# Kernel tuning notes

Measured on AMD Instinct MI355X. Metric: run time of the kernel, lower is better.

## Reference

```python
import jax, jax.numpy as jnp
import numpy as np

B, S, H = 1, 2048, 1024      # batch, seq, hidden_size
F = 4096                     # intermediate_size
E = 8                        # num_experts
K = 2                        # top-k routing


def setup_inputs() -> dict:
    key = jax.random.key(0)
    ks = jax.random.split(key, 7)
    s = 0.02  # init scale
    return {
        "x": jax.random.normal(ks[0], (B, S, H), jnp.float32),
        "gate_w": jax.random.normal(ks[1], (H, E), jnp.float32) * s,
        "gate_b": jnp.zeros((E,), jnp.float32),
        "w1": jax.random.normal(ks[2], (E, H, F), jnp.float32) * s,
        "b1": jnp.zeros((E, F), jnp.float32),
        "w2": jax.random.normal(ks[3], (E, F, H), jnp.float32) * s,
        "b2": jnp.zeros((E, H), jnp.float32),
    }


def reference(x, gate_w, gate_b, w1, b1, w2, b2):
    Bq, Sq, Hq = x.shape
    T = Bq * Sq
    xt = x.reshape(T, Hq)                              # [T,H] flatten tokens

    # --- router: softmax gate, top-k, renormalize top-k weights ---
    logits = xt @ gate_w + gate_b                      # [T,E]
    probs = jax.nn.softmax(logits, axis=-1)            # [T,E]
    top_v, top_i = jax.lax.top_k(probs, K)             # [T,K]
    top_v = top_v / jnp.sum(top_v, axis=-1, keepdims=True)
    combine = jnp.zeros((T, E), x.dtype).at[jnp.arange(T)[:, None], top_i].set(top_v)  # [T,E] sparse combine weights

    # --- experts: 2-layer FFN (ReLU), batched over experts ---
    h = jax.nn.relu(jnp.einsum('th,ehf->etf', xt, w1) + b1[:, None, :])   # [E,T,F]
    y = jnp.einsum('etf,efh->eth', h, w2) + b2[:, None, :]                # [E,T,H]

    # --- combine: weighted sum over selected experts (zeros elsewhere) ---
    out = jnp.einsum('te,eth->th', combine, y)          # [T,H]
    return out.reshape(Bq, Sq, Hq)
```

## Files before the change

kernel.cpp:

```cpp
#include <hip/hip_runtime.h>

#define TT 2048
#define HH 1024
#define FF 4096
#define EE 8
#define EROWS 640
#define ROWS_CAP 5120
#define KSPLIT2 4

typedef __bf16 bf16;
typedef bf16 bf16x8 __attribute__((ext_vector_type(8)));
typedef bf16 bf16x4 __attribute__((ext_vector_type(4)));
typedef bf16 bf16x2 __attribute__((ext_vector_type(2)));
typedef float floatx4 __attribute__((ext_vector_type(4)));

#define OFF_W1T  ((size_t)0)
#define OFF_W2T  (OFF_W1T + (size_t)67108864)
#define OFF_XG   (OFF_W2T + (size_t)67108864)
#define OFF_H    (OFF_XG  + (size_t)10485760)
#define OFF_CNT  (OFF_H   + (size_t)41943040)
#define OFF_TKW  (OFF_CNT + (size_t)256)
#define OFF_ROW  (OFF_TKW + (size_t)16384)
#define OFF_Y    OFF_W1T

__device__ __forceinline__ void gload16(const bf16* g, bf16* l) {
    __builtin_amdgcn_global_load_lds((const __attribute__((address_space(1))) void*)g,
                                     (__attribute__((address_space(3))) void*)l, 16, 0, 0);
}

__device__ __forceinline__ void raw_barrier() {
    asm volatile("s_barrier" ::: "memory");
}

__global__ __launch_bounds__(256) void transpose_cvt(const float* __restrict__ in,
                                                     bf16* __restrict__ out,
                                                     int R, int C) {
    __shared__ float tile[64][67];
    const int e  = blockIdx.z;
    const int r0 = blockIdx.y * 64, c0 = blockIdx.x * 64;
    const float* inp = in + (size_t)e * R * C;
    bf16* outp = out + (size_t)e * R * C;
    const int t = threadIdx.x;
    {
        const int lr = t >> 4;
        const int lc = (t & 15) << 2;
#pragma unroll
        for (int i = 0; i < 4; ++i) {
            int r = lr + i * 16;
            floatx4 v = __builtin_nontemporal_load(
                (const floatx4*)&inp[(size_t)(r0 + r) * C + c0 + lc]);
            tile[r][lc + 0] = v[0]; tile[r][lc + 1] = v[1];
            tile[r][lc + 2] = v[2]; tile[r][lc + 3] = v[3];
        }
    }
    __syncthreads();
    {
        const int c  = t >> 3;
        const int rq = (t & 7) << 3;
#pragma unroll
        for (int i = 0; i < 2; ++i) {
            int cc = c + i * 32;
            bf16x8 o;
#pragma unroll
            for (int k = 0; k < 8; ++k) o[k] = (bf16)tile[rq + k][cc];
            *(bf16x8*)&outp[(size_t)(c0 + cc) * R + r0 + rq] = o;
        }
    }
}

__global__ __launch_bounds__(256) void router_gather(const float* __restrict__ x,
                                                     const float* __restrict__ gw,
                                                     const float* __restrict__ gb,
                                                     int* __restrict__ counts,
                                                     bf16* __restrict__ xg,
                                                     int* __restrict__ rowOf,
                                                     float* __restrict__ tkw) {
    const int wid = blockIdx.x * 4 + (threadIdx.x >> 6);
    const int lane = threadIdx.x & 63;
    for (int t = wid; t < TT; t += 1024) {
        const float* xr = x + (size_t)t * HH;
        float xf[16];
        double acc[EE];
#pragma unroll
        for (int e = 0; e < EE; ++e) acc[e] = 0.0;
#pragma unroll
        for (int i = 0; i < 16; ++i) {
            const int h = lane + i * 64;
            const float xv = xr[h];
            xf[i] = xv;
            const float* g = gw + (size_t)h * EE;
            floatx4 g0 = *(const floatx4*)&g[0];
            floatx4 g1 = *(const floatx4*)&g[4];
            const double xd = (double)xv;
            acc[0] += xd * (double)g0[0]; acc[1] += xd * (double)g0[1];
            acc[2] += xd * (double)g0[2]; acc[3] += xd * (double)g0[3];
            acc[4] += xd * (double)g1[0]; acc[5] += xd * (double)g1[1];
            acc[6] += xd * (double)g1[2]; acc[7] += xd * (double)g1[3];
        }
#pragma unroll
        for (int e = 0; e < EE; ++e) {
            double v = acc[e];
            for (int s = 32; s > 0; s >>= 1) v += __shfl_xor(v, s, 64);
            acc[e] = v + (double)gb[e];
        }
        int row1 = 0, row2 = 0;
        if (lane == 0) {
            int i1 = 0; double v1 = acc[0];
            for (int e = 1; e < EE; ++e) if (acc[e] > v1) { v1 = acc[e]; i1 = e; }
            int i2 = -1; double v2 = -1e300;
            for (int e = 0; e < EE; ++e) if (e != i1 && acc[e] > v2) { v2 = acc[e]; i2 = e; }
            double wa = 1.0 / (1.0 + exp(v2 - v1));
            double wb = 1.0 - wa;
            int r1 = atomicAdd(&counts[i1], 1); if (r1 > EROWS - 1) r1 = EROWS - 1;
            int r2 = atomicAdd(&counts[i2], 1); if (r2 > EROWS - 1) r2 = EROWS - 1;
            row1 = i1 * EROWS + r1;
            row2 = i2 * EROWS + r2;
            rowOf[t * 2 + 0] = row1; rowOf[t * 2 + 1] = row2;
            tkw[t * 2 + 0] = (float)wa; tkw[t * 2 + 1] = (float)wb;
        }
        row1 = __shfl(row1, 0, 64);
        row2 = __shfl(row2, 0, 64);
        bf16* d1 = xg + (size_t)row1 * HH;
        bf16* d2 = xg + (size_t)row2 * HH;
#pragma unroll
        for (int i = 0; i < 16; ++i) {
            const bf16 v = (bf16)xf[i];
            d1[lane + i * 64] = v;
            d2[lane + i * 64] = v;
        }
    }
}


#define GEMM_BODY(EPILOGUE)                                                                 \
    __shared__ bf16 As[3][128 * 32];                                                        \
    __shared__ bf16 Bs[3][256 * 32];                                                        \
    const int tid = threadIdx.x;                                                            \
    const int lane = tid & 63, wave = tid >> 6;                                             \
    const int lrow = lane & 15, lq = lane >> 4;                                             \
    const int m_w = (wave & 1) << 6, n_w = (wave >> 1) << 7;                                \
    const unsigned foff = (unsigned)((lq ^ ((lrow >> 1) & 3)) << 3);                        \
    floatx4 acc[4][8];                                                                      \
    _Pragma("unroll") for (int i = 0; i < 4; ++i)                                           \
        _Pragma("unroll") for (int j = 0; j < 8; ++j)                                       \
            acc[i][j] = (floatx4){0.f, 0.f, 0.f, 0.f};                                      \
    int arow[6]; size_t gadr[6];                                                            \
    _Pragma("unroll") for (int s = 0; s < 6; ++s) {                                         \
        int c = tid + ((s < 2) ? s * 256 : (s - 2) * 256);                                  \
        int ar = c >> 2, ak = (c & 3) ^ ((ar >> 1) & 3);                                    \
        arow[s] = ar; gadr[s] = (size_t)ar * K + (size_t)ak * 8;                            \
    }                                                                                       \
    const unsigned ldsw = (unsigned)((tid & ~63) << 4);                \
                                                               \
    _Pragma("unroll") for (int p = 0; p < 2; ++p) {                                         \
        const int kb = p * 32;                                                              \
        gload16(Ab + gadr[0] + kb, (bf16*)((char*)As[p] + ldsw));                           \
        gload16(Ab + gadr[1] + kb, (bf16*)((char*)As[p] + 4096u + ldsw));                   \
        gload16(Bb + gadr[2] + kb, (bf16*)((char*)Bs[p] + ldsw));                           \
        gload16(Bb + gadr[3] + kb, (bf16*)((char*)Bs[p] + 4096u + ldsw));                   \
        gload16(Bb + gadr[4] + kb, (bf16*)((char*)Bs[p] + 8192u + ldsw));                   \
        gload16(Bb + gadr[5] + kb, (bf16*)((char*)Bs[p] + 12288u + ldsw));                  \
    }                                                                                       \
    for (int kt = 0; kt < NK; ++kt) {                                                       \
        raw_barrier();                              \
        {                                                                                   \
            const int kn = (kt + 2 < NK) ? kt + 2 : NK - 1;       \
            const int nb = (kt + 2) % 3;                                                    \
            const int kb = kn * 32;                                                         \
            gload16(Ab + gadr[0] + kb, (bf16*)((char*)As[nb] + ldsw));                      \
            gload16(Ab + gadr[1] + kb, (bf16*)((char*)As[nb] + 4096u + ldsw));              \
            gload16(Bb + gadr[2] + kb, (bf16*)((char*)Bs[nb] + ldsw));                      \
            gload16(Bb + gadr[3] + kb, (bf16*)((char*)Bs[nb] + 4096u + ldsw));              \
            gload16(Bb + gadr[4] + kb, (bf16*)((char*)Bs[nb] + 8192u + ldsw));              \
            gload16(Bb + gadr[5] + kb, (bf16*)((char*)Bs[nb] + 12288u + ldsw));             \
        }                                                                                   \
        asm volatile("s_waitcnt vmcnt(12)" ::: "memory");      \
        raw_barrier();                                               \
        const int cb = kt % 3;                                                              \
        bf16x8 af[4], bfr[8];                                                               \
        _Pragma("unroll") for (int i = 0; i < 4; ++i) {                                     \
            int m = m_w + i * 16 + lrow;                                                    \
            af[i] = *(const bf16x8*)&As[cb][(unsigned)m * 32 + foff];                       \
        }                                                                                   \
        _Pragma("unroll") for (int j = 0; j < 8; ++j) {                                     \
            int n = n_w + j * 16 + lrow;                                                    \
            bfr[j] = *(const bf16x8*)&Bs[cb][(unsigned)n * 32 + foff];                      \
        }                                                                                   \
        _Pragma("unroll") for (int i = 0; i < 4; ++i)                                       \
            _Pragma("unroll") for (int j = 0; j < 8; ++j)                                   \
                acc[i][j] = __builtin_amdgcn_mfma_f32_16x16x32_bf16(af[i], bfr[j],          \
                                                                    acc[i][j], 0, 0, 0);    \
    }                                                                                       \
    asm volatile("s_waitcnt vmcnt(0)" ::: "memory");           \
    EPILOGUE

__global__ __launch_bounds__(256, 2) void gemm1_kernel(const bf16* __restrict__ A,
                                                       const bf16* __restrict__ Bt,
                                                       const float* __restrict__ b1,
                                                       bf16* __restrict__ Hout,
                                                       const int* __restrict__ counts) {
    const int e = blockIdx.z, mt = blockIdx.y, nt = blockIdx.x;
    const int cnt = counts[e];
    if (mt * 128 >= cnt) return;
    const int row0 = e * EROWS + mt * 128;
    const int K = HH;
    const int NK = K / 32;
    const bf16* Ab = A + (size_t)row0 * K;
    const bf16* Bb = Bt + ((size_t)e * FF + (size_t)nt * 256) * K;

    GEMM_BODY({
        const float* bias = b1 + (size_t)e * FF + (size_t)nt * 256;
        bf16* Hb = Hout + (size_t)row0 * FF + (size_t)nt * 256;
        _Pragma("unroll") for (int j = 0; j < 8; ++j) {
            int col = n_w + j * 16 + lrow;
            float bv = bias[col];
            _Pragma("unroll") for (int i = 0; i < 4; ++i)
                _Pragma("unroll") for (int r = 0; r < 4; ++r) {
                    int mrow = m_w + i * 16 + (lq << 2) + r;
                    float v = acc[i][j][r] + bv;
                    Hb[(size_t)mrow * FF + col] = (bf16)(v > 0.f ? v : 0.f);
                }
        }
    })
}

__global__ __launch_bounds__(256, 2) void gemm2_kernel(const bf16* __restrict__ Hin,
                                                       const bf16* __restrict__ Bt,
                                                       const float* __restrict__ b2,
                                                       bf16* __restrict__ Y,
                                                       const int* __restrict__ counts) {
    const int e = blockIdx.z >> 2, ks = blockIdx.z & 3;
    const int mt = blockIdx.y, nt = blockIdx.x;
    const int cnt = counts[e];
    if (mt * 128 >= cnt) return;
    const int row0 = e * EROWS + mt * 128;
    const int K = FF;
    const int KC = FF / KSPLIT2;
    const int NK = KC / 32;
    const bf16* Ab = Hin + (size_t)row0 * K + ks * KC;
    const bf16* Bb = Bt + ((size_t)e * HH + (size_t)nt * 256) * K + ks * KC;

    GEMM_BODY({
        const float* bias = b2 + (size_t)e * HH + (size_t)nt * 256;
        bf16* Yb = Y + ((size_t)ks * ROWS_CAP + row0) * HH + (size_t)nt * 256;
        _Pragma("unroll") for (int j = 0; j < 8; ++j) {
            int col = n_w + j * 16 + lrow;
            float bv = (ks == 0) ? bias[col] : 0.f;
            _Pragma("unroll") for (int i = 0; i < 4; ++i)
                _Pragma("unroll") for (int r = 0; r < 4; ++r) {
                    int mrow = m_w + i * 16 + (lq << 2) + r;
                    Yb[(size_t)mrow * HH + col] = (bf16)(acc[i][j][r] + bv);
                }
        }
    })
}

__global__ __launch_bounds__(256) void combine_kernel(const bf16* __restrict__ Y,
                                                      const int* __restrict__ rowOf,
                                                      const float* __restrict__ tkw,
                                                      float* __restrict__ out) {
    const int t = blockIdx.x;
    const int tid = threadIdx.x;
    const int ra = rowOf[t * 2 + 0], rb = rowOf[t * 2 + 1];
    const float wa = tkw[t * 2 + 0], wb = tkw[t * 2 + 1];
    const int c = tid * 4;
    float acc[4] = {0.f, 0.f, 0.f, 0.f};
#pragma unroll
    for (int ks = 0; ks < KSPLIT2; ++ks) {
        bf16x4 a = *(const bf16x4*)&Y[((size_t)ks * ROWS_CAP + ra) * HH + c];
        bf16x4 b = *(const bf16x4*)&Y[((size_t)ks * ROWS_CAP + rb) * HH + c];
#pragma unroll
        for (int k = 0; k < 4; ++k) acc[k] += wa * (float)a[k] + wb * (float)b[k];
    }
    floatx4 o; o[0] = acc[0]; o[1] = acc[1]; o[2] = acc[2]; o[3] = acc[3];
    *(floatx4*)&out[(size_t)t * HH + c] = o;
}

extern "C" void kernel_launch(void* const* d_in, const int* in_sizes, int n_in,
                              void* d_out, int out_size, void* d_ws, size_t ws_size,
                              hipStream_t stream) {
    const float* x  = (const float*)d_in[0];
    const float* gw = (const float*)d_in[1];
    const float* gb = (const float*)d_in[2];
    const float* w1 = (const float*)d_in[3];
    const float* b1 = (const float*)d_in[4];
    const float* w2 = (const float*)d_in[5];
    const float* b2 = (const float*)d_in[6];
    float* out = (float*)d_out;
    char* ws = (char*)d_ws;

    bf16*  w1t  = (bf16*)(ws + OFF_W1T);
    bf16*  w2t  = (bf16*)(ws + OFF_W2T);
    bf16*  xg   = (bf16*)(ws + OFF_XG);
    bf16*  hbuf = (bf16*)(ws + OFF_H);
    bf16*  ybuf = (bf16*)(ws + OFF_Y);
    int*   cnts = (int*)(ws + OFF_CNT);
    float* tkw  = (float*)(ws + OFF_TKW);
    int*   rowOf= (int*)(ws + OFF_ROW);

    hipMemsetAsync(cnts, 0, 256, stream);

    router_gather<<<256, 256, 0, stream>>>(x, gw, gb, cnts, xg, rowOf, tkw);
    transpose_cvt<<<dim3(FF / 64, HH / 64, EE), 256, 0, stream>>>(w1, w1t, HH, FF);
    transpose_cvt<<<dim3(HH / 64, FF / 64, EE), 256, 0, stream>>>(w2, w2t, FF, HH);
    gemm1_kernel<<<dim3(FF / 256, 5, EE), 256, 0, stream>>>(xg, w1t, b1, hbuf, cnts);
    gemm2_kernel<<<dim3(HH / 256, 5, EE * KSPLIT2), 256, 0, stream>>>(hbuf, w2t, b2, ybuf, cnts);
    combine_kernel<<<TT, 256, 0, stream>>>(ybuf, rowOf, tkw, out);
}
```

Before: 492.1 us.

## Fuse fp32 weight transpose-convert into GEMM B-tile loading

Removes the two separate transpose_cvt kernels that converted fp32 w1/w2 to transposed bf16 in the workspace. Each GEMM now reads fp32 weights directly through registers, converts them to bf16 and writes them swizzled into LDS. The pipeline changes from a 3-stage async global_load_lds ring to a 2-stage register-prefetch double buffer with __syncthreads. This saves a full read and write pass over 512MB of weights per call, but the GEMMs now read twice as many bytes of B and each M-tile block re-reads and re-converts the same weights, with shallower latency hiding.

After: 619.6 us. 1.26x slower.

```diff
diff --git a/kernel.cpp b/kernel.cpp
--- a/kernel.cpp
+++ b/kernel.cpp
@@ -14,58 +14,16 @@
 typedef bf16 bf16x2 __attribute__((ext_vector_type(2)));
 typedef float floatx4 __attribute__((ext_vector_type(4)));
 
-#define OFF_W1T  ((size_t)0)
-#define OFF_W2T  (OFF_W1T + (size_t)67108864)
-#define OFF_XG   (OFF_W2T + (size_t)67108864)
+#define OFF_XG   ((size_t)0)
 #define OFF_H    (OFF_XG  + (size_t)10485760)
-#define OFF_CNT  (OFF_H   + (size_t)41943040)
+#define OFF_Y    (OFF_H   + (size_t)41943040)
+#define OFF_CNT  (OFF_Y   + (size_t)41943040)
 #define OFF_TKW  (OFF_CNT + (size_t)256)
 #define OFF_ROW  (OFF_TKW + (size_t)16384)
-#define OFF_Y    OFF_W1T
 
 __device__ __forceinline__ void gload16(const bf16* g, bf16* l) {
     __builtin_amdgcn_global_load_lds((const __attribute__((address_space(1))) void*)g,
                                      (__attribute__((address_space(3))) void*)l, 16, 0, 0);
-}
-
-__device__ __forceinline__ void raw_barrier() {
-    asm volatile("s_barrier" ::: "memory");
-}
-
-__global__ __launch_bounds__(256) void transpose_cvt(const float* __restrict__ in,
-                                                     bf16* __restrict__ out,
-                                                     int R, int C) {
-    __shared__ float tile[64][67];
-    const int e  = blockIdx.z;
-    const int r0 = blockIdx.y * 64, c0 = blockIdx.x * 64;
-    const float* inp = in + (size_t)e * R * C;
-    bf16* outp = out + (size_t)e * R * C;
-    const int t = threadIdx.x;
-    {
-        const int lr = t >> 4;
-        const int lc = (t & 15) << 2;
-#pragma unroll
-        for (int i = 0; i < 4; ++i) {
-            int r = lr + i * 16;
-            floatx4 v = __builtin_nontemporal_load(
-                (const floatx4*)&inp[(size_t)(r0 + r) * C + c0 + lc]);
-            tile[r][lc + 0] = v[0]; tile[r][lc + 1] = v[1];
-            tile[r][lc + 2] = v[2]; tile[r][lc + 3] = v[3];
-        }
-    }
-    __syncthreads();
-    {
-        const int c  = t >> 3;
-        const int rq = (t & 7) << 3;
-#pragma unroll
-        for (int i = 0; i < 2; ++i) {
-            int cc = c + i * 32;
-            bf16x8 o;
-#pragma unroll
-            for (int k = 0; k < 8; ++k) o[k] = (bf16)tile[rq + k][cc];
-            *(bf16x8*)&outp[(size_t)(c0 + cc) * R + r0 + rq] = o;
-        }
-    }
 }
 
 __global__ __launch_bounds__(256) void router_gather(const float* __restrict__ x,
@@ -132,9 +90,34 @@
 }
 
 
+#define B_LOAD(KT) do {                                                                     \
+        const float* bp = bsrc + (size_t)(KT) * 32 * LDB;                                   \
+        _Pragma("unroll") for (int q = 0; q < 4; ++q) {                                     \
+            bv[q]     = *(const floatx4*)(bp + q * 4);                                      \
+            bv[4 + q] = *(const floatx4*)(bp + LDB + q * 4);                                \
+        }                                                                                   \
+    } while (0)
+
+#define B_WRITE(ST) do {                                                                    \
+        bf16* bb = &Bs[ST][(unsigned)nb * 512 + ((unsigned)(kp & 3) << 1)];                 \
+        const int bq = kp >> 2;                                                             \
+        _Pragma("unroll") for (int j = 0; j < 16; ++j) {                                    \
+            bf16x2 p;                                                                       \
+            p[0] = (bf16)bv[j >> 2][j & 3];                                                 \
+            p[1] = (bf16)bv[4 + (j >> 2)][j & 3];                                           \
+            *(bf16x2*)(bb + j * 32 + ((unsigned)(bq ^ ((j >> 1) & 3)) << 3)) = p;           \
+        }                                                                                   \
+    } while (0)
+
+#define A_STAGE(KT, ST) do {                                                                \
+        const int kb = (KT) * 32;                                                           \
+        gload16(Ab + agadr0 + kb, (bf16*)((char*)As[ST] + ldsw));                           \
+        gload16(Ab + agadr1 + kb, (bf16*)((char*)As[ST] + 4096u + ldsw));                   \
+    } while (0)
+
 #define GEMM_BODY(EPILOGUE)                                                                 \
-    __shared__ bf16 As[3][128 * 32];                                                        \
-    __shared__ bf16 Bs[3][256 * 32];                                                        \
+    __shared__ bf16 As[2][128 * 32];                                                        \
+    __shared__ bf16 Bs[2][256 * 32];                                                        \
     const int tid = threadIdx.x;                                                            \
     const int lane = tid & 63, wave = tid >> 6;                                             \
     const int lrow = lane & 15, lq = lane >> 4;                                             \
@@ -144,39 +127,28 @@
     _Pragma("unroll") for (int i = 0; i < 4; ++i)                                           \
         _Pragma("unroll") for (int j = 0; j < 8; ++j)                                       \
             acc[i][j] = (floatx4){0.f, 0.f, 0.f, 0.f};                                      \
-    int arow[6]; size_t gadr[6];                                                            \
-    _Pragma("unroll") for (int s = 0; s < 6; ++s) {                                         \
-        int c = tid + ((s < 2) ? s * 256 : (s - 2) * 256);                                  \
-        int ar = c >> 2, ak = (c & 3) ^ ((ar >> 1) & 3);                                    \
-        arow[s] = ar; gadr[s] = (size_t)ar * K + (size_t)ak * 8;                            \
+    size_t agadr0, agadr1;                                                                  \
+    {                                                                                       \
+        int c0 = tid, ar0 = c0 >> 2, ak0 = (c0 & 3) ^ ((ar0 >> 1) & 3);                     \
+        agadr0 = (size_t)ar0 * LDA + (size_t)ak0 * 8;                                       \
+        int c1 = tid + 256, ar1 = c1 >> 2, ak1 = (c1 & 3) ^ ((ar1 >> 1) & 3);               \
+        agadr1 = (size_t)ar1 * LDA + (size_t)ak1 * 8;                                       \
     }                                                                                       \
     const unsigned ldsw = (unsigned)((tid & ~63) << 4);                \
-                                                               \
-    _Pragma("unroll") for (int p = 0; p < 2; ++p) {                                         \
-        const int kb = p * 32;                                                              \
-        gload16(Ab + gadr[0] + kb, (bf16*)((char*)As[p] + ldsw));                           \
-        gload16(Ab + gadr[1] + kb, (bf16*)((char*)As[p] + 4096u + ldsw));                   \
-        gload16(Bb + gadr[2] + kb, (bf16*)((char*)Bs[p] + ldsw));                           \
-        gload16(Bb + gadr[3] + kb, (bf16*)((char*)Bs[p] + 4096u + ldsw));                   \
-        gload16(Bb + gadr[4] + kb, (bf16*)((char*)Bs[p] + 8192u + ldsw));                   \
-        gload16(Bb + gadr[5] + kb, (bf16*)((char*)Bs[p] + 12288u + ldsw));                  \
-    }                                                                                       \
+    const int kp = tid & 15, nb = tid >> 4;                                                 \
+    const float* bsrc = Bf + (size_t)(2 * kp) * LDB + (size_t)nb * 16;                      \
+    floatx4 bv[8];                                                                          \
+                                                  \
+    B_LOAD(0);                                                                              \
+    A_STAGE(0, 0);                                                                          \
+    B_WRITE(0);                                                                             \
+    __syncthreads();                                                                        \
     for (int kt = 0; kt < NK; ++kt) {                                                       \
-        raw_barrier();                              \
-        {                                                                                   \
-            const int kn = (kt + 2 < NK) ? kt + 2 : NK - 1;       \
-            const int nb = (kt + 2) % 3;                                                    \
-            const int kb = kn * 32;                                                         \
-            gload16(Ab + gadr[0] + kb, (bf16*)((char*)As[nb] + ldsw));                      \
-            gload16(Ab + gadr[1] + kb, (bf16*)((char*)As[nb] + 4096u + ldsw));              \
-            gload16(Bb + gadr[2] + kb, (bf16*)((char*)Bs[nb] + ldsw));                      \
-            gload16(Bb + gadr[3] + kb, (bf16*)((char*)Bs[nb] + 4096u + ldsw));              \
-            gload16(Bb + gadr[4] + kb, (bf16*)((char*)Bs[nb] + 8192u + ldsw));              \
-            gload16(Bb + gadr[5] + kb, (bf16*)((char*)Bs[nb] + 12288u + ldsw));             \
-        }                                                                                   \
-        asm volatile("s_waitcnt vmcnt(12)" ::: "memory");      \
-        raw_barrier();                                               \
-        const int cb = kt % 3;                                                              \
+        const int cb = kt & 1;                                                              \
+        if (kt + 1 < NK) {                                                                  \
+            B_LOAD(kt + 1);                         \
+            A_STAGE(kt + 1, cb ^ 1);                          \
+        }                                                                                   \
         bf16x8 af[4], bfr[8];                                                               \
         _Pragma("unroll") for (int i = 0; i < 4; ++i) {                                     \
             int m = m_w + i * 16 + lrow;                                                    \
@@ -190,12 +162,13 @@
             _Pragma("unroll") for (int j = 0; j < 8; ++j)                                   \
                 acc[i][j] = __builtin_amdgcn_mfma_f32_16x16x32_bf16(af[i], bfr[j],          \
                                                                     acc[i][j], 0, 0, 0);    \
+        if (kt + 1 < NK) B_WRITE(cb ^ 1);                                                   \
+        __syncthreads();        \
     }                                                                                       \
-    asm volatile("s_waitcnt vmcnt(0)" ::: "memory");           \
     EPILOGUE
 
 __global__ __launch_bounds__(256, 2) void gemm1_kernel(const bf16* __restrict__ A,
-                                                       const bf16* __restrict__ Bt,
+                                                       const float* __restrict__ W1,
                                                        const float* __restrict__ b1,
                                                        bf16* __restrict__ Hout,
                                                        const int* __restrict__ counts) {
@@ -203,21 +176,22 @@
     const int cnt = counts[e];
     if (mt * 128 >= cnt) return;
     const int row0 = e * EROWS + mt * 128;
-    const int K = HH;
-    const int NK = K / 32;
-    const bf16* Ab = A + (size_t)row0 * K;
-    const bf16* Bb = Bt + ((size_t)e * FF + (size_t)nt * 256) * K;
+    const int LDA = HH;
+    const int LDB = FF;
+    const int NK = HH / 32;
+    const bf16*  Ab = A + (size_t)row0 * LDA;
+    const float* Bf = W1 + (size_t)e * HH * FF + (size_t)nt * 256;
 
     GEMM_BODY({
         const float* bias = b1 + (size_t)e * FF + (size_t)nt * 256;
         bf16* Hb = Hout + (size_t)row0 * FF + (size_t)nt * 256;
         _Pragma("unroll") for (int j = 0; j < 8; ++j) {
             int col = n_w + j * 16 + lrow;
-            float bv = bias[col];
+            float bv_ = bias[col];
             _Pragma("unroll") for (int i = 0; i < 4; ++i)
                 _Pragma("unroll") for (int r = 0; r < 4; ++r) {
                     int mrow = m_w + i * 16 + (lq << 2) + r;
-                    float v = acc[i][j][r] + bv;
+                    float v = acc[i][j][r] + bv_;
                     Hb[(size_t)mrow * FF + col] = (bf16)(v > 0.f ? v : 0.f);
                 }
         }
@@ -225,7 +199,7 @@
 }
 
 __global__ __launch_bounds__(256, 2) void gemm2_kernel(const bf16* __restrict__ Hin,
-                                                       const bf16* __restrict__ Bt,
+                                                       const float* __restrict__ W2,
                                                        const float* __restrict__ b2,
                                                        bf16* __restrict__ Y,
                                                        const int* __restrict__ counts) {
@@ -234,22 +208,23 @@
     const int cnt = counts[e];
     if (mt * 128 >= cnt) return;
     const int row0 = e * EROWS + mt * 128;
-    const int K = FF;
     const int KC = FF / KSPLIT2;
+    const int LDA = FF;
+    const int LDB = HH;
     const int NK = KC / 32;
-    const bf16* Ab = Hin + (size_t)row0 * K + ks * KC;
-    const bf16* Bb = Bt + ((size_t)e * HH + (size_t)nt * 256) * K + ks * KC;
+    const bf16*  Ab = Hin + (size_t)row0 * LDA + ks * KC;
+    const float* Bf = W2 + (size_t)e * FF * HH + (size_t)(ks * KC) * HH + (size_t)nt * 256;
 
     GEMM_BODY({
         const float* bias = b2 + (size_t)e * HH + (size_t)nt * 256;
         bf16* Yb = Y + ((size_t)ks * ROWS_CAP + row0) * HH + (size_t)nt * 256;
         _Pragma("unroll") for (int j = 0; j < 8; ++j) {
             int col = n_w + j * 16 + lrow;
-            float bv = (ks == 0) ? bias[col] : 0.f;
+            float bv_ = (ks == 0) ? bias[col] : 0.f;
             _Pragma("unroll") for (int i = 0; i < 4; ++i)
                 _Pragma("unroll") for (int r = 0; r < 4; ++r) {
                     int mrow = m_w + i * 16 + (lq << 2) + r;
-                    Yb[(size_t)mrow * HH + col] = (bf16)(acc[i][j][r] + bv);
+                    Yb[(size_t)mrow * HH + col] = (bf16)(acc[i][j][r] + bv_);
                 }
         }
     })
@@ -289,8 +264,6 @@
     float* out = (float*)d_out;
     char* ws = (char*)d_ws;
 
-    bf16*  w1t  = (bf16*)(ws + OFF_W1T);
-    bf16*  w2t  = (bf16*)(ws + OFF_W2T);
     bf16*  xg   = (bf16*)(ws + OFF_XG);
     bf16*  hbuf = (bf16*)(ws + OFF_H);
     bf16*  ybuf = (bf16*)(ws + OFF_Y);
@@ -301,9 +274,7 @@
     hipMemsetAsync(cnts, 0, 256, stream);
 
     router_gather<<<256, 256, 0, stream>>>(x, gw, gb, cnts, xg, rowOf, tkw);
-    transpose_cvt<<<dim3(FF / 64, HH / 64, EE), 256, 0, stream>>>(w1, w1t, HH, FF);
-    transpose_cvt<<<dim3(HH / 64, FF / 64, EE), 256, 0, stream>>>(w2, w2t, FF, HH);
-    gemm1_kernel<<<dim3(FF / 256, 5, EE), 256, 0, stream>>>(xg, w1t, b1, hbuf, cnts);
-    gemm2_kernel<<<dim3(HH / 256, 5, EE * KSPLIT2), 256, 0, stream>>>(hbuf, w2t, b2, ybuf, cnts);
+    gemm1_kernel<<<dim3(FF / 256, 5, EE), 256, 0, stream>>>(xg, w1, b1, hbuf, cnts);
+    gemm2_kernel<<<dim3(HH / 256, 5, EE * KSPLIT2), 256, 0, stream>>>(hbuf, w2, b2, ybuf, cnts);
     combine_kernel<<<TT, 256, 0, stream>>>(ybuf, rowOf, tkw, out);
 }
```

## Switch GEMMs to double-buffered LDS and raise occupancy to three blocks per CU

Applied to the files above, without the earlier changes.

Cuts the LDS ring in both expert GEMMs from three stages to two, so each iteration prefetches one tile ahead and waits with vmcnt(6). Launch bounds rise from 2 to 3 blocks per CU so more waves can hide latency. The catch is a shallower prefetch, and the register cap of 3 blocks with 128 fp32 accumulators per thread could cause spills.

Result: slower. 587.0 us (+19.3%).

```diff
diff --git a/kernel.cpp b/kernel.cpp
--- a/kernel.cpp
+++ b/kernel.cpp
@@ -132,9 +132,19 @@
 }
 
 
+#define STAGE(KT, ST) do {                                                                  \
+        const int kb = (KT) * 32;                                                           \
+        gload16(Ab + gadr[0] + kb, (bf16*)((char*)As[ST] + ldsw));                          \
+        gload16(Ab + gadr[1] + kb, (bf16*)((char*)As[ST] + 4096u + ldsw));                  \
+        gload16(Bb + gadr[2] + kb, (bf16*)((char*)Bs[ST] + ldsw));                          \
+        gload16(Bb + gadr[3] + kb, (bf16*)((char*)Bs[ST] + 4096u + ldsw));                  \
+        gload16(Bb + gadr[4] + kb, (bf16*)((char*)Bs[ST] + 8192u + ldsw));                  \
+        gload16(Bb + gadr[5] + kb, (bf16*)((char*)Bs[ST] + 12288u + ldsw));                 \
+    } while (0)
+
 #define GEMM_BODY(EPILOGUE)                                                                 \
-    __shared__ bf16 As[3][128 * 32];                                                        \
-    __shared__ bf16 Bs[3][256 * 32];                                                        \
+    __shared__ bf16 As[2][128 * 32];                                                        \
+    __shared__ bf16 Bs[2][256 * 32];                                                        \
     const int tid = threadIdx.x;                                                            \
     const int lane = tid & 63, wave = tid >> 6;                                             \
     const int lrow = lane & 15, lq = lane >> 4;                                             \
@@ -151,32 +161,17 @@
         arow[s] = ar; gadr[s] = (size_t)ar * K + (size_t)ak * 8;                            \
     }                                                                                       \
     const unsigned ldsw = (unsigned)((tid & ~63) << 4);                \
-                                                               \
-    _Pragma("unroll") for (int p = 0; p < 2; ++p) {                                         \
-        const int kb = p * 32;                                                              \
-        gload16(Ab + gadr[0] + kb, (bf16*)((char*)As[p] + ldsw));                           \
-        gload16(Ab + gadr[1] + kb, (bf16*)((char*)As[p] + 4096u + ldsw));                   \
-        gload16(Bb + gadr[2] + kb, (bf16*)((char*)Bs[p] + ldsw));                           \
-        gload16(Bb + gadr[3] + kb, (bf16*)((char*)Bs[p] + 4096u + ldsw));                   \
-        gload16(Bb + gadr[4] + kb, (bf16*)((char*)Bs[p] + 8192u + ldsw));                   \
-        gload16(Bb + gadr[5] + kb, (bf16*)((char*)Bs[p] + 12288u + ldsw));                  \
-    }                                                                                       \
+                                                  \
+    STAGE(0, 0);                                                                            \
     for (int kt = 0; kt < NK; ++kt) {                                                       \
-        raw_barrier();                              \
+        const int cb = kt & 1;                                                              \
+        raw_barrier();              \
         {                                                                                   \
-            const int kn = (kt + 2 < NK) ? kt + 2 : NK - 1;       \
-            const int nb = (kt + 2) % 3;                                                    \
-            const int kb = kn * 32;                                                         \
-            gload16(Ab + gadr[0] + kb, (bf16*)((char*)As[nb] + ldsw));                      \
-            gload16(Ab + gadr[1] + kb, (bf16*)((char*)As[nb] + 4096u + ldsw));              \
-            gload16(Bb + gadr[2] + kb, (bf16*)((char*)Bs[nb] + ldsw));                      \
-            gload16(Bb + gadr[3] + kb, (bf16*)((char*)Bs[nb] + 4096u + ldsw));              \
-            gload16(Bb + gadr[4] + kb, (bf16*)((char*)Bs[nb] + 8192u + ldsw));              \
-            gload16(Bb + gadr[5] + kb, (bf16*)((char*)Bs[nb] + 12288u + ldsw));             \
+            const int kn = (kt + 1 < NK) ? kt + 1 : NK - 1;       \
+            STAGE(kn, cb ^ 1);                                                              \
         }                                                                                   \
-        asm volatile("s_waitcnt vmcnt(12)" ::: "memory");      \
+        asm volatile("s_waitcnt vmcnt(6)" ::: "memory");       \
         raw_barrier();                                               \
-        const int cb = kt % 3;                                                              \
         bf16x8 af[4], bfr[8];                                                               \
         _Pragma("unroll") for (int i = 0; i < 4; ++i) {                                     \
             int m = m_w + i * 16 + lrow;                                                    \
@@ -194,7 +189,7 @@
     asm volatile("s_waitcnt vmcnt(0)" ::: "memory");           \
     EPILOGUE
 
-__global__ __launch_bounds__(256, 2) void gemm1_kernel(const bf16* __restrict__ A,
+__global__ __launch_bounds__(256, 3) void gemm1_kernel(const bf16* __restrict__ A,
                                                        const bf16* __restrict__ Bt,
                                                        const float* __restrict__ b1,
                                                        bf16* __restrict__ Hout,
@@ -224,7 +219,7 @@
     })
 }
 
-__global__ __launch_bounds__(256, 2) void gemm2_kernel(const bf16* __restrict__ Hin,
+__global__ __launch_bounds__(256, 3) void gemm2_kernel(const bf16* __restrict__ Hin,
                                                        const bf16* __restrict__ Bt,
                                                        const float* __restrict__ b2,
                                                        bf16* __restrict__ Y,
```
